# Performance work log

Measured on AMD Instinct MI355X. Metric: run time of the kernel, lower is better.

## Reference

```python
import jax, jax.numpy as jnp
import numpy as np

B, C, L, H, W = 8, 768, 8, 14, 14
HEADS = 12
HD = C // HEADS
SCALE = HD ** (-0.5)
KQ, SQ, PQ = (3, 3, 3), (1, 1, 1), (1, 1, 1)
KKV, SKV, PKV = (3, 3, 3), (1, 2, 2), (1, 1, 1)
EPS = 1e-6


def setup_inputs() -> dict:
    key = jax.random.key(0)
    ks = jax.random.split(key, 16)
    s = 0.02
    inp = {
        'x': jax.random.normal(ks[0], (B, C, L, H, W), jnp.float32),
        'class_token': jax.random.normal(ks[1], (B, C), jnp.float32),
        'Wq': jax.random.normal(ks[2], (C, C), jnp.float32) * s,
        'bq': jnp.zeros((C,), jnp.float32),
        'Wk': jax.random.normal(ks[3], (C, C), jnp.float32) * s,
        'bk': jnp.zeros((C,), jnp.float32),
        'Wv': jax.random.normal(ks[4], (C, C), jnp.float32) * s,
        'bv': jnp.zeros((C,), jnp.float32),
        # depthwise Conv3d kernels: (C, 1, kD, kH, kW), groups=C, no bias
        'conv_q': jax.random.normal(ks[5], (C, 1) + KQ, jnp.float32) * 0.1,
        'conv_k': jax.random.normal(ks[6], (C, 1) + KKV, jnp.float32) * 0.1,
        'conv_v': jax.random.normal(ks[7], (C, 1) + KKV, jnp.float32) * 0.1,
        'lnq_w': jnp.ones((C,), jnp.float32), 'lnq_b': jnp.zeros((C,), jnp.float32),
        'lnk_w': jnp.ones((C,), jnp.float32), 'lnk_b': jnp.zeros((C,), jnp.float32),
        'lnv_w': jnp.ones((C,), jnp.float32), 'lnv_b': jnp.zeros((C,), jnp.float32),
        'Wproj': jax.random.normal(ks[8], (C, C), jnp.float32) * s,
        'bproj': jnp.zeros((C,), jnp.float32),
    }
    return inp


def _linear_keep(x, cls, Wm, b):
    # x: (B,C,l,h,w) -> tokens (B,N,C), prepend cls, linear, split
    Bb, Cc, l, h, w = x.shape
    t = x.reshape(Bb, Cc, -1).transpose(0, 2, 1)          # (B,N,C)
    t = jnp.concatenate([cls[:, None, :], t], axis=1)      # (B,1+N,C)
    y = t @ Wm.T + b
    cls_o = y[:, 0]
    y = y[:, 1:].transpose(0, 2, 1).reshape(Bb, -1, l, h, w)
    return y, cls_o


def _pool(x, wconv, stride, pad, ln_w, ln_b):
    # depthwise 3D conv (groups=C), then LayerNorm over channels
    y = jax.lax.conv_general_dilated(
        x, wconv, window_strides=stride,
        padding=[(p, p) for p in pad],
        dimension_numbers=('NCDHW', 'OIDHW', 'NCDHW'),
        feature_group_count=C)
    y = jnp.moveaxis(y, 1, -1)                            # (B,l,h,w,C)
    mu = y.mean(-1, keepdims=True)
    var = y.var(-1, keepdims=True)
    y = (y - mu) * jax.lax.rsqrt(var + EPS) * ln_w + ln_b
    return jnp.moveaxis(y, -1, 1)


def _to_heads(t):
    # (B,C,l,h,w) -> (B,heads,N,head_dim)
    Bb = t.shape[0]
    return t.reshape(Bb, HEADS, HD, -1).transpose(0, 1, 3, 2)


def _attention(q, k, v, cq, ck, cv, Wp, bp, out_lhw):
    Bb = q.shape[0]
    q = jnp.concatenate([cq.reshape(Bb, HEADS, 1, HD), _to_heads(q)], axis=2)
    k = jnp.concatenate([ck.reshape(Bb, HEADS, 1, HD), _to_heads(k)], axis=2)
    v = jnp.concatenate([cv.reshape(Bb, HEADS, 1, HD), _to_heads(v)], axis=2)
    scores = jnp.einsum('bhqc,bhkc->bhqk', q, k) * SCALE
    attn = jax.nn.softmax(scores, axis=-1)
    o = jnp.einsum('bhqk,bhkc->bhqc', attn, v)            # (B,heads,1+Nq,hd)
    o = o.transpose(0, 2, 1, 3).reshape(Bb, -1, C)        # (B,1+Nq,C)
    o = o @ Wp.T + bp
    cls_o = o[:, 0]
    xo = o[:, 1:].transpose(0, 2, 1).reshape(Bb, C, *out_lhw)
    return xo, cls_o


def reference(x, class_token, Wq, bq, Wk, bk, Wv, bv,
              conv_q, conv_k, conv_v,
              lnq_w, lnq_b, lnk_w, lnk_b, lnv_w, lnv_b,
              Wproj, bproj):
    # pool_first=False: QKV linears first (with cls token), then pooling of the
    # spatial tensors only (cls tokens bypass pooling).
    q, cls_q = _linear_keep(x, class_token, Wq, bq)
    k, cls_k = _linear_keep(x, class_token, Wk, bk)
    v, cls_v = _linear_keep(x, class_token, Wv, bv)
    q = _pool(q, conv_q, SQ, PQ, lnq_w, lnq_b)
    k = _pool(k, conv_k, SKV, PKV, lnk_w, lnk_b)
    v = _pool(v, conv_v, SKV, PKV, lnv_w, lnv_b)
    out_lhw = q.shape[2:]
    return _attention(q, k, v, cls_q, cls_k, cls_v, Wproj, bproj, out_lhw)
```

## Files before the change

### kernel.cpp

```cpp
#include <hip/hip_runtime.h>

#define CDIM 768
#define BATCH 8
#define LDEPTH 8
#define HHEIGHT 14
#define WWIDTH 14
#define NSP 1568
#define NSPX 1576
#define NQTOK 1569
#define NKSP 392
#define NKTOK 393
#define NHEADS 12
#define HEADDIM 64
#define ATTN_SCALE 0.125f
#define LN_EPS 1e-6f
#define MTOK (BATCH * NQTOK)
#define NPAD_X 1792
#define NPAD_TOK 12800
#define WELEM (CDIM * CDIM)
#define TQP 1664
#define TKP 448

typedef _Float16 f16;
typedef _Float16 f16x8_t __attribute__((ext_vector_type(8)));
typedef _Float16 f16x4_t __attribute__((ext_vector_type(4)));
typedef float f32x4_t __attribute__((ext_vector_type(4)));

__device__ __forceinline__ void gld_lds16(const void* g, void* l) {
  __builtin_amdgcn_global_load_lds(
      (const __attribute__((address_space(1))) void*)g,
      (__attribute__((address_space(3))) void*)l, 16, 0, 0);
}

__global__ __launch_bounds__(256) void convert4_kernel(
    const float* __restrict__ s0, const float* __restrict__ s1,
    const float* __restrict__ s2, const float* __restrict__ s3,
    f16* __restrict__ dst) {
  const int mat = blockIdx.y;
  const float* src = (mat == 0) ? s0 : (mat == 1) ? s1 : (mat == 2) ? s2 : s3;
  int i = (blockIdx.x * 256 + threadIdx.x) * 4;
  if (i < WELEM) {
    float4 v = *(const float4*)&src[i];
    f16x4_t h = {(f16)v.x, (f16)v.y, (f16)v.z, (f16)v.w};
    *(f16x4_t*)&dst[(size_t)mat * WELEM + i] = h;
  }
}

__global__ __launch_bounds__(256) void transpose_x_kernel(
    const float* __restrict__ X, const float* __restrict__ cls,
    f16* __restrict__ Xt) {
  __shared__ float t[32][33];
  const int b = blockIdx.z;
  const int k0 = blockIdx.y * 32;
  const int n0 = blockIdx.x * 32;
  const int tx = threadIdx.x & 31, ty = threadIdx.x >> 5;
#pragma unroll
  for (int i = 0; i < 4; i++) {
    int k = k0 + ty + i * 8;
    int n = n0 + tx;
    float v;
    if (n < NSP)
      v = X[((size_t)b * CDIM + k) * NSP + n];
    else if (n == NSP)
      v = cls[b * CDIM + k];
    else
      v = 0.f;
    t[ty + i * 8][tx] = v;
  }
  __syncthreads();
#pragma unroll
  for (int i = 0; i < 4; i++) {
    int n = n0 + ty + i * 8;
    Xt[((size_t)b * NPAD_X + n) * CDIM + k0 + tx] = (f16)t[tx][ty + i * 8];
  }
}

__global__ __launch_bounds__(256, 2) void gemm_qkv_f16_kernel(
    const f16* __restrict__ W16, const f16* __restrict__ Xt,
    const float* __restrict__ bq, const float* __restrict__ bk,
    const float* __restrict__ bv, f16* __restrict__ OutBase) {
  __shared__ __align__(16) f16 Asm[128 * 32];
  __shared__ __align__(16) f16 Bsm[256 * 32];

  const int bid = blockIdx.x;
  const int b = bid & 7;
  const int rem = bid >> 3;
  const int mat = rem / 42;
  const int rem2 = rem % 42;
  const int m0 = (rem2 / 7) * 128;
  const int n0 = (rem2 % 7) * 256;
  const int tid = threadIdx.x;
  const int lane = tid & 63;
  const int w = tid >> 6;
  const int wr = w >> 1, wc = w & 1;
  const int l15 = lane & 15, l4 = lane >> 4;

  const f16* A16 = W16 + (size_t)mat * WELEM;
  const float* bias = (mat == 0) ? bq : (mat == 1) ? bk : bv;
  f16* Out = OutBase + (size_t)mat * ((size_t)BATCH * CDIM * NSPX);

  const int srow = lane >> 2;
  const int skq = ((lane & 3) ^ ((lane >> 3) & 3)) * 8;
  const f16* Ag = A16 + (size_t)(m0 + w * 32 + srow) * CDIM + skq;
  const f16* Bg = Xt + ((size_t)b * NPAD_X + n0 + w * 64 + srow) * CDIM + skq;
  f16* lA = Asm + w * 32 * 32;
  f16* lB = Bsm + w * 64 * 32;

  const int rsw = (l15 >> 1) & 3;
  const int kchunk = (l4 ^ rsw) * 8;

  f32x4_t acc[4][8];
#pragma unroll
  for (int i = 0; i < 4; i++)
#pragma unroll
    for (int j = 0; j < 8; j++) acc[i][j] = (f32x4_t){0.f, 0.f, 0.f, 0.f};

  for (int k0 = 0; k0 < CDIM; k0 += 32) {
    gld_lds16(Ag + k0, lA);
    gld_lds16(Ag + 16 * CDIM + k0, lA + 16 * 32);
    gld_lds16(Bg + k0, lB);
    gld_lds16(Bg + 16 * CDIM + k0, lB + 16 * 32);
    gld_lds16(Bg + 32 * CDIM + k0, lB + 32 * 32);
    gld_lds16(Bg + 48 * CDIM + k0, lB + 48 * 32);
    __syncthreads();
    f16x8_t af[4];
#pragma unroll
    for (int mi = 0; mi < 4; mi++)
      af[mi] = *(const f16x8_t*)(Asm + (wr * 64 + mi * 16 + l15) * 32 + kchunk);
#pragma unroll
    for (int ni = 0; ni < 8; ni++) {
      f16x8_t bfv =
          *(const f16x8_t*)(Bsm + (wc * 128 + ni * 16 + l15) * 32 + kchunk);
#pragma unroll
      for (int mi = 0; mi < 4; mi++)
        acc[mi][ni] = __builtin_amdgcn_mfma_f32_16x16x32_f16(
            af[mi], bfv, acc[mi][ni], 0, 0, 0);
    }
    __syncthreads();
  }

#pragma unroll
  for (int mi = 0; mi < 4; mi++) {
    const int mbase = m0 + wr * 64 + mi * 16 + l4 * 4;
#pragma unroll
    for (int ni = 0; ni < 8; ni++) {
      const int n = n0 + wc * 128 + ni * 16 + l15;
      if (n < NQTOK) {
#pragma unroll
        for (int r = 0; r < 4; r++) {
          Out[((size_t)b * CDIM + mbase + r) * NSPX + n] =
              (f16)(acc[mi][ni][r] + bias[mbase + r]);
        }
      }
    }
  }
}

__global__ __launch_bounds__(256, 2) void gemm_proj_f16_kernel(
    const f16* __restrict__ Wp16, const f16* __restrict__ o16,
    const float* __restrict__ bias, float* __restrict__ xo,
    float* __restrict__ cls_o) {
  __shared__ __align__(16) f16 Asm[128 * 32];
  __shared__ __align__(16) f16 Bsm[256 * 32];

  const int bid = blockIdx.x;
  const int xcd = bid & 7, pos_ = bid >> 3;
  const int base = (xcd < 4) ? xcd * 38 : 152 + (xcd - 4) * 37;
  const int wgid = base + pos_;
  const int m0 = (wgid / 50) * 128;
  const int n0 = (wgid % 50) * 256;
  const int tid = threadIdx.x;
  const int lane = tid & 63;
  const int w = tid >> 6;
  const int wr = w >> 1, wc = w & 1;
  const int l15 = lane & 15, l4 = lane >> 4;

  const int srow = lane >> 2;
  const int skq = ((lane & 3) ^ ((lane >> 3) & 3)) * 8;
  const f16* Ag = Wp16 + (size_t)(m0 + srow) * CDIM + skq;
  const f16* Bg = o16 + (size_t)(n0 + w * 64 + srow) * CDIM + skq;
  f16* lA = Asm + w * 32 * 32;
  f16* lB = Bsm + w * 64 * 32;
  const f16* Agw = Ag + (size_t)(w * 32) * CDIM;

  const int rsw = (l15 >> 1) & 3;
  const int kchunk = (l4 ^ rsw) * 8;

  f32x4_t acc[4][8];
#pragma unroll
  for (int i = 0; i < 4; i++)
#pragma unroll
    for (int j = 0; j < 8; j++) acc[i][j] = (f32x4_t){0.f, 0.f, 0.f, 0.f};

  for (int k0 = 0; k0 < CDIM; k0 += 32) {
    gld_lds16(Agw + k0, lA);
    gld_lds16(Agw + 16 * CDIM + k0, lA + 16 * 32);
    gld_lds16(Bg + k0, lB);
    gld_lds16(Bg + 16 * CDIM + k0, lB + 16 * 32);
    gld_lds16(Bg + 32 * CDIM + k0, lB + 32 * 32);
    gld_lds16(Bg + 48 * CDIM + k0, lB + 48 * 32);
    __syncthreads();
    f16x8_t af[4];
#pragma unroll
    for (int mi = 0; mi < 4; mi++)
      af[mi] = *(const f16x8_t*)(Asm + (wr * 64 + mi * 16 + l15) * 32 + kchunk);
#pragma unroll
    for (int ni = 0; ni < 8; ni++) {
      f16x8_t bfv =
          *(const f16x8_t*)(Bsm + (wc * 128 + ni * 16 + l15) * 32 + kchunk);
#pragma unroll
      for (int mi = 0; mi < 4; mi++)
        acc[mi][ni] = __builtin_amdgcn_mfma_f32_16x16x32_f16(
            af[mi], bfv, acc[mi][ni], 0, 0, 0);
    }
    __syncthreads();
  }

#pragma unroll
  for (int ni = 0; ni < 8; ni++) {
    const int tok = n0 + wc * 128 + ni * 16 + l15;
    if (tok < MTOK) {
      const int bb = tok / NQTOK;
      const int nn = tok % NQTOK;
#pragma unroll
      for (int mi = 0; mi < 4; mi++) {
        const int mbase = m0 + wr * 64 + mi * 16 + l4 * 4;
#pragma unroll
        for (int r = 0; r < 4; r++) {
          float v = acc[mi][ni][r] + bias[mbase + r];
          if (nn == 0)
            cls_o[bb * CDIM + mbase + r] = v;
          else
            xo[((size_t)bb * CDIM + mbase + r) * (size_t)NSP + nn - 1] = v;
        }
      }
    }
  }
}

__global__ __launch_bounds__(256) void dwconv_kernel(
    const f16* __restrict__ X, const float* __restrict__ wconv,
    f16* __restrict__ Out, int Lo, int Ho, int Wo, int sh, int sw,
    int istride) {
  __shared__ float xin[NSP];
  __shared__ float wsm[27];
  const int c = blockIdx.x % CDIM;
  const int b = blockIdx.x / CDIM;
  const f16* xb = X + ((size_t)b * CDIM + c) * (size_t)istride;
  for (int i = threadIdx.x * 8; i < NSP; i += 2048) {
    f16x8_t v = *(const f16x8_t*)&xb[i];
#pragma unroll
    for (int j = 0; j < 8; j++) xin[i + j] = (float)v[j];
  }
  if (threadIdx.x < 27) wsm[threadIdx.x] = wconv[c * 27 + threadIdx.x];
  __syncthreads();
  const int npos = Lo * Ho * Wo;
  f16* ob = Out + ((size_t)b * CDIM + c) * (size_t)npos;
  for (int pos = threadIdx.x; pos < npos; pos += 256) {
    int wo = pos % Wo;
    int ho = (pos / Wo) % Ho;
    int lo = pos / (Wo * Ho);
    int li0 = lo - 1, hi0 = ho * sh - 1, wi0 = wo * sw - 1;
    float sum = 0.f;
#pragma unroll
    for (int kd = 0; kd < 3; kd++) {
      int li = li0 + kd;
      if (li < 0 || li >= LDEPTH) continue;
#pragma unroll
      for (int kh = 0; kh < 3; kh++) {
        int hi = hi0 + kh;
        if (hi < 0 || hi >= HHEIGHT) continue;
#pragma unroll
        for (int kw = 0; kw < 3; kw++) {
          int wi = wi0 + kw;
          if (wi < 0 || wi >= WWIDTH) continue;
          sum = fmaf(xin[(li * HHEIGHT + hi) * WWIDTH + wi],
                     wsm[(kd * 3 + kh) * 3 + kw], sum);
        }
      }
    }
    ob[pos] = (f16)sum;
  }
}

__global__ __launch_bounds__(256) void ln_pack_qk_kernel(
    const f16* __restrict__ xp, const float* __restrict__ ln_w,
    const float* __restrict__ ln_b, f16* __restrict__ OutH, int np, int tp) {
  const int b = blockIdx.y;
  const int p0 = blockIdx.x * 32;
  const int tid = threadIdx.x;
  const int pl = tid & 31;
  const int grp = tid >> 5;
  const int pos = p0 + pl;
  const bool act = pos < np;
  const f16* Xb = xp + (size_t)b * CDIM * (size_t)np;

  __shared__ __align__(16) f16 tile[32][784];
  __shared__ float r1[8][33], r2[8][33];
  __shared__ float smean[32], srstd[32];

  const int swz = (pl & 7) << 3;
  float s1 = 0.f, s2 = 0.f;
  for (int cc = 0; cc < 12; cc++) {
    const int c0 = grp * 96 + cc * 8;
    f16x8_t hv;
#pragma unroll
    for (int i = 0; i < 8; i++) {
      f16 h = act ? Xb[(size_t)(c0 + i) * np + pos] : (f16)0.f;
      hv[i] = h;
      float v = (float)h;
      s1 += v;
      s2 = fmaf(v, v, s2);
    }
    *(f16x8_t*)&tile[pl][c0 ^ swz] = hv;
  }
  r1[grp][pl] = s1;
  r2[grp][pl] = s2;
  __syncthreads();
  if (tid < 32) {
    float t1 = 0.f, t2 = 0.f;
#pragma unroll
    for (int g = 0; g < 8; g++) { t1 += r1[g][tid]; t2 += r2[g][tid]; }
    float mean = t1 * (1.f / 768.f);
    float var = t2 * (1.f / 768.f) - mean * mean;
    smean[tid] = mean;
    srstd[tid] = rsqrtf(var + LN_EPS);
  }
  __syncthreads();

  const int tl = tid >> 3, d8 = (tid & 7) * 8;
  const float mean = smean[tl], rstd = srstd[tl];
  const bool wv = (p0 + tl) < np;
  const int tswz = (tl & 7) << 3;
#pragma unroll
  for (int h = 0; h < NHEADS; h++) {
    const int c = h * 64 + d8;
    f16x8_t raw = *(const f16x8_t*)&tile[tl][c ^ tswz];
    float4 w1 = *(const float4*)&ln_w[c];
    float4 w2 = *(const float4*)&ln_w[c + 4];
    float4 b1 = *(const float4*)&ln_b[c];
    float4 b2 = *(const float4*)&ln_b[c + 4];
    f16x8_t ov;
    ov[0] = (f16)(((float)raw[0] - mean) * rstd * w1.x + b1.x);
    ov[1] = (f16)(((float)raw[1] - mean) * rstd * w1.y + b1.y);
    ov[2] = (f16)(((float)raw[2] - mean) * rstd * w1.z + b1.z);
    ov[3] = (f16)(((float)raw[3] - mean) * rstd * w1.w + b1.w);
    ov[4] = (f16)(((float)raw[4] - mean) * rstd * w2.x + b2.x);
    ov[5] = (f16)(((float)raw[5] - mean) * rstd * w2.y + b2.y);
    ov[6] = (f16)(((float)raw[6] - mean) * rstd * w2.z + b2.z);
    ov[7] = (f16)(((float)raw[7] - mean) * rstd * w2.w + b2.w);
    if (wv)
      *(uint4*)(OutH +
                (((size_t)(b * NHEADS + h)) * (size_t)tp + (p0 + tl + 1)) * 64 +
                d8) = *(uint4*)&ov;
  }
}

__global__ __launch_bounds__(256) void ln_pack_v_kernel(
    const f16* __restrict__ vp, const f16* __restrict__ vlin,
    const float* __restrict__ ln_w, const float* __restrict__ ln_b,
    f16* __restrict__ Vht) {
  const int b = blockIdx.y;
  const int t0 = blockIdx.x * 32;
  const int tid = threadIdx.x;
  const int pl = tid & 31;
  const int grp = tid >> 5;
  const int t = t0 + pl;
  const int pos = t - 1;
  const bool isv = (t >= 1) && (t < NKTOK);
  const f16* Vb = vp + (size_t)b * CDIM * (size_t)NKSP;

  __shared__ float r1[8][33], r2[8][33];
  __shared__ float smean[32], srstd[32];
  __shared__ __align__(16) f16 vtile[128][40];

  float s1 = 0.f, s2 = 0.f;
  if (isv) {
    for (int c = grp; c < CDIM; c += 8) {
      float v = (float)Vb[(size_t)c * NKSP + pos];
      s1 += v;
      s2 = fmaf(v, v, s2);
    }
  }
  r1[grp][pl] = s1;
  r2[grp][pl] = s2;
  __syncthreads();
  if (tid < 32) {
    float t1 = 0.f, t2 = 0.f;
#pragma unroll
    for (int g = 0; g < 8; g++) { t1 += r1[g][tid]; t2 += r2[g][tid]; }
    float mean = t1 * (1.f / 768.f);
    float var = t2 * (1.f / 768.f) - mean * mean;
    smean[tid] = mean;
    srstd[tid] = rsqrtf(var + LN_EPS);
  }
  __syncthreads();
  const float mean = smean[pl], rstd = srstd[pl];

  for (int cc = 0; cc < 6; cc++) {
#pragma unroll
    for (int i = 0; i < 16; i++) {
      int cl = grp * 16 + i;
      int c = cc * 128 + cl;
      float outv;
      if (isv)
        outv = ((float)Vb[(size_t)c * NKSP + pos] - mean) * rstd * ln_w[c] +
               ln_b[c];
      else if (t == 0)
        outv = (float)vlin[((size_t)b * CDIM + c) * NSPX + NSP];
      else
        outv = 0.f;
      vtile[cl][pl] = (f16)outv;
    }
    __syncthreads();
#pragma unroll
    for (int it = 0; it < 2; it++) {
      int idx = it * 256 + tid;
      int cl = idx >> 2, t8 = (idx & 3) * 8;
      uint4 vv = *(const uint4*)&vtile[cl][t8];
      *(uint4*)(Vht + ((size_t)b * CDIM + cc * 128 + cl) * (size_t)TKP + t0 +
                t8) = vv;
    }
    __syncthreads();
  }
}

__global__ __launch_bounds__(768) void cls_fill_kernel(
    const f16* __restrict__ qlin, const f16* __restrict__ klin,
    f16* __restrict__ Qh, f16* __restrict__ Kh) {
  const int b = blockIdx.x;
  const int c = threadIdx.x;
  Qh[(((size_t)(b * NHEADS + (c >> 6))) * TQP) * 64 + (c & 63)] =
      qlin[((size_t)b * CDIM + c) * NSPX + NSP];
  Kh[(((size_t)(b * NHEADS + (c >> 6))) * TKP) * 64 + (c & 63)] =
      klin[((size_t)b * CDIM + c) * NSPX + NSP];
}

__global__ __launch_bounds__(256) void attn_mfma_kernel(
    const f16* __restrict__ Qh, const f16* __restrict__ Kh,
    const f16* __restrict__ Vht, f16* __restrict__ o16) {
  __shared__ __align__(16) f16 Ks[64 * 72];
  __shared__ __align__(16) f16 Vt[64 * 72];
  const int qt = blockIdx.x, h = blockIdx.y, b = blockIdx.z;
  const int tid = threadIdx.x;
  const int lane = tid & 63;
  const int w = tid >> 6;
  const int l15 = lane & 15, l4 = lane >> 4;
  const int q0 = qt * 128 + w * 32;

  const f16* Qp = Qh + ((size_t)(b * NHEADS + h) * TQP) * 64;
  const f16* Kp = Kh + ((size_t)(b * NHEADS + h) * TKP) * 64;
  const f16* Vp = Vht + ((size_t)(b * NHEADS + h) * 64) * TKP;

  f16x8_t bq[2][2];
#pragma unroll
  for (int qi = 0; qi < 2; qi++)
#pragma unroll
    for (int kf = 0; kf < 2; kf++)
      bq[qi][kf] = *(const f16x8_t*)(Qp + (size_t)(q0 + qi * 16 + l15) * 64 +
                                     kf * 32 + l4 * 8);

  f32x4_t oacc[4][2];
#pragma unroll
  for (int df = 0; df < 4; df++)
#pragma unroll
    for (int qi = 0; qi < 2; qi++) oacc[df][qi] = (f32x4_t){0.f, 0.f, 0.f, 0.f};
  float mrow[2] = {-1e30f, -1e30f};
  float lrow[2] = {0.f, 0.f};

  const int sr = tid >> 2, sc = (tid & 3) * 16;

  for (int kv0 = 0; kv0 < TKP; kv0 += 64) {
    const f16* kg = Kp + (size_t)(kv0 + sr) * 64 + sc;
    uint4 kl0 = *(const uint4*)kg;
    uint4 kl1 = *(const uint4*)(kg + 8);
    const f16* vg = Vp + (size_t)sr * TKP + kv0 + sc;
    uint4 vl0 = *(const uint4*)vg;
    uint4 vl1 = *(const uint4*)(vg + 8);
    __syncthreads();
    *(uint4*)(Ks + sr * 72 + sc) = kl0;
    *(uint4*)(Ks + sr * 72 + sc + 8) = kl1;
    *(uint4*)(Vt + sr * 72 + sc) = vl0;
    *(uint4*)(Vt + sr * 72 + sc + 8) = vl1;
    __syncthreads();

    f32x4_t sacc[4][2];
#pragma unroll
    for (int ki = 0; ki < 4; ki++)
#pragma unroll
      for (int qi = 0; qi < 2; qi++) sacc[ki][qi] = (f32x4_t){0.f, 0.f, 0.f, 0.f};
#pragma unroll
    for (int kf = 0; kf < 2; kf++) {
#pragma unroll
      for (int ki = 0; ki < 4; ki++) {
        f16x8_t ak =
            *(const f16x8_t*)(Ks + (ki * 16 + l15) * 72 + kf * 32 + l4 * 8);
#pragma unroll
        for (int qi = 0; qi < 2; qi++)
          sacc[ki][qi] = __builtin_amdgcn_mfma_f32_16x16x32_f16(
              ak, bq[qi][kf], sacc[ki][qi], 0, 0, 0);
      }
    }

    float pmax[2] = {-1e30f, -1e30f};
#pragma unroll
    for (int ki = 0; ki < 4; ki++) {
      const int keyb = kv0 + ki * 16 + l4 * 4;
#pragma unroll
      for (int qi = 0; qi < 2; qi++) {
#pragma unroll
        for (int rr = 0; rr < 4; rr++) {
          float s = sacc[ki][qi][rr] * ATTN_SCALE;
          if (keyb + rr >= NKTOK) s = -1e30f;
          sacc[ki][qi][rr] = s;
          pmax[qi] = fmaxf(pmax[qi], s);
        }
      }
    }
#pragma unroll
    for (int qi = 0; qi < 2; qi++) {
      pmax[qi] = fmaxf(pmax[qi], __shfl_xor(pmax[qi], 16, 64));
      pmax[qi] = fmaxf(pmax[qi], __shfl_xor(pmax[qi], 32, 64));
      float mnew = fmaxf(mrow[qi], pmax[qi]);
      float alpha = __expf(mrow[qi] - mnew);
      mrow[qi] = mnew;
      lrow[qi] *= alpha;
#pragma unroll
      for (int df = 0; df < 4; df++) {
        oacc[df][qi][0] *= alpha;
        oacc[df][qi][1] *= alpha;
        oacc[df][qi][2] *= alpha;
        oacc[df][qi][3] *= alpha;
      }
    }
    f16x4_t pb[4][2];
#pragma unroll
    for (int ki = 0; ki < 4; ki++) {
#pragma unroll
      for (int qi = 0; qi < 2; qi++) {
        float p0 = __expf(sacc[ki][qi][0] - mrow[qi]);
        float p1 = __expf(sacc[ki][qi][1] - mrow[qi]);
        float p2 = __expf(sacc[ki][qi][2] - mrow[qi]);
        float p3 = __expf(sacc[ki][qi][3] - mrow[qi]);
        lrow[qi] += p0 + p1 + p2 + p3;
        f16x4_t pv = {(f16)p0, (f16)p1, (f16)p2, (f16)p3};
        pb[ki][qi] = pv;
      }
    }

#pragma unroll
    for (int df = 0; df < 4; df++) {
#pragma unroll
      for (int ki = 0; ki < 4; ki++) {
        f16x4_t av =
            *(const f16x4_t*)(Vt + (df * 16 + l15) * 72 + ki * 16 + l4 * 4);
#pragma unroll
        for (int qi = 0; qi < 2; qi++)
          oacc[df][qi] = __builtin_amdgcn_mfma_f32_16x16x16f16(
              av, pb[ki][qi], oacc[df][qi], 0, 0, 0);
      }
    }
  }

  float inv[2];
#pragma unroll
  for (int qi = 0; qi < 2; qi++) {
    float l = lrow[qi];
    l += __shfl_xor(l, 16, 64);
    l += __shfl_xor(l, 32, 64);
    inv[qi] = 1.f / l;
  }
#pragma unroll
  for (int qi = 0; qi < 2; qi++) {
    const int q = q0 + qi * 16 + l15;
    if (q < NQTOK) {
      f16* op = o16 + ((size_t)(b * NQTOK + q)) * CDIM + h * 64 + l4 * 4;
#pragma unroll
      for (int df = 0; df < 4; df++) {
        f16x4_t ov = {(f16)(oacc[df][qi][0] * inv[qi]),
                      (f16)(oacc[df][qi][1] * inv[qi]),
                      (f16)(oacc[df][qi][2] * inv[qi]),
                      (f16)(oacc[df][qi][3] * inv[qi])};
        *(f16x4_t*)(op + df * 16) = ov;
      }
    }
  }
}

extern "C" void kernel_launch(void* const* d_in, const int* in_sizes, int n_in,
                              void* d_out, int out_size, void* d_ws, size_t ws_size,
                              hipStream_t stream) {
  const float* x      = (const float*)d_in[0];
  const float* cls    = (const float*)d_in[1];
  const float* Wq     = (const float*)d_in[2];
  const float* bq     = (const float*)d_in[3];
  const float* Wk     = (const float*)d_in[4];
  const float* bk     = (const float*)d_in[5];
  const float* Wv     = (const float*)d_in[6];
  const float* bv     = (const float*)d_in[7];
  const float* conv_q = (const float*)d_in[8];
  const float* conv_k = (const float*)d_in[9];
  const float* conv_v = (const float*)d_in[10];
  const float* lnq_w  = (const float*)d_in[11];
  const float* lnq_b  = (const float*)d_in[12];
  const float* lnk_w  = (const float*)d_in[13];
  const float* lnk_b  = (const float*)d_in[14];
  const float* lnv_w  = (const float*)d_in[15];
  const float* lnv_b  = (const float*)d_in[16];
  const float* Wproj  = (const float*)d_in[17];
  const float* bproj  = (const float*)d_in[18];

  char* wsb = (char*)d_ws;
  f16*   Xt     = (f16*)(wsb + 0);
  f16*   W16    = (f16*)(wsb + 22020096);
  f16*   q_lin  = (f16*)(wsb + 26738688);
  f16*   k_lin  = (f16*)(wsb + 46104576);
  f16*   v_lin  = (f16*)(wsb + 65470464);
  f16*   k_pool = (f16*)(wsb + 84836352);
  f16*   v_pool = (f16*)(wsb + 89653248);
  f16*   Kh     = (f16*)(wsb + 94470144);
  f16*   Vht    = (f16*)(wsb + 99975168);
  f16*   q_pool = k_lin;
  f16*   Qh     = Xt;
  f16*   o16    = v_lin;

  f16* W16p = W16 + (size_t)3 * WELEM;

  convert4_kernel<<<dim3(576, 4), 256, 0, stream>>>(Wq, Wk, Wv, Wproj, W16);

  transpose_x_kernel<<<dim3(56, 24, BATCH), 256, 0, stream>>>(x, cls, Xt);

  gemm_qkv_f16_kernel<<<1008, 256, 0, stream>>>(W16, Xt, bq, bk, bv, q_lin);

  dwconv_kernel<<<BATCH * CDIM, 256, 0, stream>>>(k_lin, conv_k, k_pool,
                                                  8, 7, 7, 2, 2, NSPX);
  dwconv_kernel<<<BATCH * CDIM, 256, 0, stream>>>(v_lin, conv_v, v_pool,
                                                  8, 7, 7, 2, 2, NSPX);
  cls_fill_kernel<<<BATCH, 768, 0, stream>>>(q_lin, k_lin, Qh, Kh);
  dwconv_kernel<<<BATCH * CDIM, 256, 0, stream>>>(q_lin, conv_q, q_pool,
                                                  8, 14, 14, 1, 1, NSPX);

  ln_pack_qk_kernel<<<dim3(49, BATCH), 256, 0, stream>>>(q_pool, lnq_w, lnq_b,
                                                         Qh, NSP, TQP);
  ln_pack_qk_kernel<<<dim3(13, BATCH), 256, 0, stream>>>(k_pool, lnk_w, lnk_b,
                                                         Kh, NKSP, TKP);
  ln_pack_v_kernel<<<dim3(14, BATCH), 256, 0, stream>>>(v_pool, v_lin, lnv_w,
                                                        lnv_b, Vht);

  attn_mfma_kernel<<<dim3(13, NHEADS, BATCH), 256, 0, stream>>>(Qh, Kh, Vht,
                                                                o16);

  float* xo = (float*)d_out;
  float* cls_o = (float*)d_out + (size_t)BATCH * CDIM * NSP;
  gemm_proj_f16_kernel<<<300, 256, 0, stream>>>(W16p, o16, bproj, xo, cls_o);
}
```

Before: 355.9 us.

## Merge dwconv and LN-pack launches, enlarge attention query tile to 256

The three depthwise conv launches become one grid with a y-dimension selecting q/k/v, and the two Q/K layernorm-pack launches merge into one grid. Because q_pool gets its own workspace buffer, the q conv no longer has to wait for the k conv to finish with k_lin. The attention kernel now handles 64 queries per wave (256 per block), so each K/V tile staged in LDS is reused by twice as many queries, and Q padding grows to 1792 to match. In exchange the attention kernel uses more registers, which can lower occupancy, and its grid shrinks from 13 to 7 query tiles.

```diff
diff --git a/kernel.cpp b/kernel.cpp
--- a/kernel.cpp
+++ b/kernel.cpp
@@ -16,9 +16,8 @@
 #define LN_EPS 1e-6f
 #define MTOK (BATCH * NQTOK)
 #define NPAD_X 1792
-#define NPAD_TOK 12800
 #define WELEM (CDIM * CDIM)
-#define TQP 1664
+#define TQP 1792
 #define TKP 448
 
 typedef _Float16 f16;
@@ -238,15 +237,23 @@
   }
 }
 
-__global__ __launch_bounds__(256) void dwconv_kernel(
-    const f16* __restrict__ X, const float* __restrict__ wconv,
-    f16* __restrict__ Out, int Lo, int Ho, int Wo, int sh, int sw,
-    int istride) {
+__global__ __launch_bounds__(256) void dwconv3_kernel(
+    const f16* __restrict__ q_lin, const f16* __restrict__ k_lin,
+    const f16* __restrict__ v_lin, const float* __restrict__ cq,
+    const float* __restrict__ ck, const float* __restrict__ cv,
+    f16* __restrict__ q_pool, f16* __restrict__ k_pool,
+    f16* __restrict__ v_pool) {
   __shared__ float xin[NSP];
   __shared__ float wsm[27];
+  const int which = blockIdx.y;
+  const f16* X = (which == 0) ? k_lin : (which == 1) ? v_lin : q_lin;
+  const float* wconv = (which == 0) ? ck : (which == 1) ? cv : cq;
+  f16* Out = (which == 0) ? k_pool : (which == 1) ? v_pool : q_pool;
+  const int Ho = (which == 2) ? 14 : 7;
+  const int s = (which == 2) ? 1 : 2;
   const int c = blockIdx.x % CDIM;
   const int b = blockIdx.x / CDIM;
-  const f16* xb = X + ((size_t)b * CDIM + c) * (size_t)istride;
+  const f16* xb = X + ((size_t)b * CDIM + c) * (size_t)NSPX;
   for (int i = threadIdx.x * 8; i < NSP; i += 2048) {
     f16x8_t v = *(const f16x8_t*)&xb[i];
 #pragma unroll
@@ -254,13 +261,13 @@
   }
   if (threadIdx.x < 27) wsm[threadIdx.x] = wconv[c * 27 + threadIdx.x];
   __syncthreads();
-  const int npos = Lo * Ho * Wo;
+  const int npos = 8 * Ho * Ho;
   f16* ob = Out + ((size_t)b * CDIM + c) * (size_t)npos;
   for (int pos = threadIdx.x; pos < npos; pos += 256) {
-    int wo = pos % Wo;
-    int ho = (pos / Wo) % Ho;
-    int lo = pos / (Wo * Ho);
-    int li0 = lo - 1, hi0 = ho * sh - 1, wi0 = wo * sw - 1;
+    int wo = pos % Ho;
+    int ho = (pos / Ho) % Ho;
+    int lo = pos / (Ho * Ho);
+    int li0 = lo - 1, hi0 = ho * s - 1, wi0 = wo * s - 1;
     float sum = 0.f;
 #pragma unroll
     for (int kd = 0; kd < 3; kd++) {
@@ -283,11 +290,21 @@
   }
 }
 
-__global__ __launch_bounds__(256) void ln_pack_qk_kernel(
-    const f16* __restrict__ xp, const float* __restrict__ ln_w,
-    const float* __restrict__ ln_b, f16* __restrict__ OutH, int np, int tp) {
+__global__ __launch_bounds__(256) void ln_pack_qk2_kernel(
+    const f16* __restrict__ qp, const f16* __restrict__ kp,
+    const float* __restrict__ lnq_w, const float* __restrict__ lnq_b,
+    const float* __restrict__ lnk_w, const float* __restrict__ lnk_b,
+    f16* __restrict__ Qh, f16* __restrict__ Kh) {
+  const int bx = blockIdx.x;
+  const bool isq = bx < 49;
+  const f16* xp = isq ? qp : kp;
+  const float* ln_w = isq ? lnq_w : lnk_w;
+  const float* ln_b = isq ? lnq_b : lnk_b;
+  f16* OutH = isq ? Qh : Kh;
+  const int np = isq ? NSP : NKSP;
+  const int tp = isq ? TQP : TKP;
   const int b = blockIdx.y;
-  const int p0 = blockIdx.x * 32;
+  const int p0 = (isq ? bx : bx - 49) * 32;
   const int tid = threadIdx.x;
   const int pl = tid & 31;
   const int grp = tid >> 5;
@@ -446,27 +463,27 @@
   const int lane = tid & 63;
   const int w = tid >> 6;
   const int l15 = lane & 15, l4 = lane >> 4;
-  const int q0 = qt * 128 + w * 32;
+  const int q0 = qt * 256 + w * 64;
 
   const f16* Qp = Qh + ((size_t)(b * NHEADS + h) * TQP) * 64;
   const f16* Kp = Kh + ((size_t)(b * NHEADS + h) * TKP) * 64;
   const f16* Vp = Vht + ((size_t)(b * NHEADS + h) * 64) * TKP;
 
-  f16x8_t bq[2][2];
-#pragma unroll
-  for (int qi = 0; qi < 2; qi++)
+  f16x8_t bq[4][2];
+#pragma unroll
+  for (int qi = 0; qi < 4; qi++)
 #pragma unroll
     for (int kf = 0; kf < 2; kf++)
       bq[qi][kf] = *(const f16x8_t*)(Qp + (size_t)(q0 + qi * 16 + l15) * 64 +
                                      kf * 32 + l4 * 8);
 
-  f32x4_t oacc[4][2];
+  f32x4_t oacc[4][4];
 #pragma unroll
   for (int df = 0; df < 4; df++)
 #pragma unroll
-    for (int qi = 0; qi < 2; qi++) oacc[df][qi] = (f32x4_t){0.f, 0.f, 0.f, 0.f};
-  float mrow[2] = {-1e30f, -1e30f};
-  float lrow[2] = {0.f, 0.f};
+    for (int qi = 0; qi < 4; qi++) oacc[df][qi] = (f32x4_t){0.f, 0.f, 0.f, 0.f};
+  float mrow[4] = {-1e30f, -1e30f, -1e30f, -1e30f};
+  float lrow[4] = {0.f, 0.f, 0.f, 0.f};
 
   const int sr = tid >> 2, sc = (tid & 3) * 16;
 
@@ -484,11 +501,12 @@
     *(uint4*)(Vt + sr * 72 + sc + 8) = vl1;
     __syncthreads();
 
-    f32x4_t sacc[4][2];
+    f32x4_t sacc[4][4];
 #pragma unroll
     for (int ki = 0; ki < 4; ki++)
 #pragma unroll
-      for (int qi = 0; qi < 2; qi++) sacc[ki][qi] = (f32x4_t){0.f, 0.f, 0.f, 0.f};
+      for (int qi = 0; qi < 4; qi++)
+        sacc[ki][qi] = (f32x4_t){0.f, 0.f, 0.f, 0.f};
 #pragma unroll
     for (int kf = 0; kf < 2; kf++) {
 #pragma unroll
@@ -496,18 +514,18 @@
         f16x8_t ak =
             *(const f16x8_t*)(Ks + (ki * 16 + l15) * 72 + kf * 32 + l4 * 8);
 #pragma unroll
-        for (int qi = 0; qi < 2; qi++)
+        for (int qi = 0; qi < 4; qi++)
           sacc[ki][qi] = __builtin_amdgcn_mfma_f32_16x16x32_f16(
               ak, bq[qi][kf], sacc[ki][qi], 0, 0, 0);
       }
     }
 
-    float pmax[2] = {-1e30f, -1e30f};
+    float pmax[4] = {-1e30f, -1e30f, -1e30f, -1e30f};
 #pragma unroll
     for (int ki = 0; ki < 4; ki++) {
       const int keyb = kv0 + ki * 16 + l4 * 4;
 #pragma unroll
-      for (int qi = 0; qi < 2; qi++) {
+      for (int qi = 0; qi < 4; qi++) {
 #pragma unroll
         for (int rr = 0; rr < 4; rr++) {
           float s = sacc[ki][qi][rr] * ATTN_SCALE;
@@ -518,7 +536,7 @@
       }
     }
 #pragma unroll
-    for (int qi = 0; qi < 2; qi++) {
+    for (int qi = 0; qi < 4; qi++) {
       pmax[qi] = fmaxf(pmax[qi], __shfl_xor(pmax[qi], 16, 64));
       pmax[qi] = fmaxf(pmax[qi], __shfl_xor(pmax[qi], 32, 64));
       float mnew = fmaxf(mrow[qi], pmax[qi]);
@@ -533,45 +551,42 @@
         oacc[df][qi][3] *= alpha;
       }
     }
-    f16x4_t pb[4][2];
+
 #pragma unroll
     for (int ki = 0; ki < 4; ki++) {
-#pragma unroll
-      for (int qi = 0; qi < 2; qi++) {
+      f16x4_t pb[4];
+#pragma unroll
+      for (int qi = 0; qi < 4; qi++) {
         float p0 = __expf(sacc[ki][qi][0] - mrow[qi]);
         float p1 = __expf(sacc[ki][qi][1] - mrow[qi]);
         float p2 = __expf(sacc[ki][qi][2] - mrow[qi]);
         float p3 = __expf(sacc[ki][qi][3] - mrow[qi]);
         lrow[qi] += p0 + p1 + p2 + p3;
         f16x4_t pv = {(f16)p0, (f16)p1, (f16)p2, (f16)p3};
-        pb[ki][qi] = pv;
-      }
-    }
-
-#pragma unroll
-    for (int df = 0; df < 4; df++) {
-#pragma unroll
-      for (int ki = 0; ki < 4; ki++) {
+        pb[qi] = pv;
+      }
+#pragma unroll
+      for (int df = 0; df < 4; df++) {
         f16x4_t av =
             *(const f16x4_t*)(Vt + (df * 16 + l15) * 72 + ki * 16 + l4 * 4);
 #pragma unroll
-        for (int qi = 0; qi < 2; qi++)
+        for (int qi = 0; qi < 4; qi++)
           oacc[df][qi] = __builtin_amdgcn_mfma_f32_16x16x16f16(
-              av, pb[ki][qi], oacc[df][qi], 0, 0, 0);
-      }
-    }
-  }
-
-  float inv[2];
-#pragma unroll
-  for (int qi = 0; qi < 2; qi++) {
+              av, pb[qi], oacc[df][qi], 0, 0, 0);
+      }
+    }
+  }
+
+  float inv[4];
+#pragma unroll
+  for (int qi = 0; qi < 4; qi++) {
     float l = lrow[qi];
     l += __shfl_xor(l, 16, 64);
     l += __shfl_xor(l, 32, 64);
     inv[qi] = 1.f / l;
   }
 #pragma unroll
-  for (int qi = 0; qi < 2; qi++) {
+  for (int qi = 0; qi < 4; qi++) {
     const int q = q0 + qi * 16 + l15;
     if (q < NQTOK) {
       f16* op = o16 + ((size_t)(b * NQTOK + q)) * CDIM + h * 64 + l4 * 4;
@@ -620,7 +635,7 @@
   f16*   v_pool = (f16*)(wsb + 89653248);
   f16*   Kh     = (f16*)(wsb + 94470144);
   f16*   Vht    = (f16*)(wsb + 99975168);
-  f16*   q_pool = k_lin;
+  f16*   q_pool = (f16*)(wsb + 105480192);
   f16*   Qh     = Xt;
   f16*   o16    = v_lin;
 
@@ -632,23 +647,18 @@
 
   gemm_qkv_f16_kernel<<<1008, 256, 0, stream>>>(W16, Xt, bq, bk, bv, q_lin);
 
-  dwconv_kernel<<<BATCH * CDIM, 256, 0, stream>>>(k_lin, conv_k, k_pool,
-                                                  8, 7, 7, 2, 2, NSPX);
-  dwconv_kernel<<<BATCH * CDIM, 256, 0, stream>>>(v_lin, conv_v, v_pool,
-                                                  8, 7, 7, 2, 2, NSPX);
   cls_fill_kernel<<<BATCH, 768, 0, stream>>>(q_lin, k_lin, Qh, Kh);
-  dwconv_kernel<<<BATCH * CDIM, 256, 0, stream>>>(q_lin, conv_q, q_pool,
-                                                  8, 14, 14, 1, 1, NSPX);
-
-  ln_pack_qk_kernel<<<dim3(49, BATCH), 256, 0, stream>>>(q_pool, lnq_w, lnq_b,
-                                                         Qh, NSP, TQP);
-  ln_pack_qk_kernel<<<dim3(13, BATCH), 256, 0, stream>>>(k_pool, lnk_w, lnk_b,
-                                                         Kh, NKSP, TKP);
+
+  dwconv3_kernel<<<dim3(BATCH * CDIM, 3), 256, 0, stream>>>(
+      q_lin, k_lin, v_lin, conv_q, conv_k, conv_v, q_pool, k_pool, v_pool);
+
+  ln_pack_qk2_kernel<<<dim3(62, BATCH), 256, 0, stream>>>(
+      q_pool, k_pool, lnq_w, lnq_b, lnk_w, lnk_b, Qh, Kh);
   ln_pack_v_kernel<<<dim3(14, BATCH), 256, 0, stream>>>(v_pool, v_lin, lnv_w,
                                                         lnv_b, Vht);
 
-  attn_mfma_kernel<<<dim3(13, NHEADS, BATCH), 256, 0, stream>>>(Qh, Kh, Vht,
-                                                                o16);
+  attn_mfma_kernel<<<dim3(7, NHEADS, BATCH), 256, 0, stream>>>(Qh, Kh, Vht,
+                                                               o16);
 
   float* xo = (float*)d_out;
   float* cls_o = (float*)d_out + (size_t)BATCH * CDIM * NSP;
```

Result: no change. 352.9 us (-0.9%).
